# Kernel tuning notes

Measured on AMD Instinct MI355X. Metric: run time of the kernel, lower is better.

Reference implementation:

```python
import jax, jax.numpy as jnp
import numpy as np

N_NODES = 100000
N_EDGES = 1600000
N_GRAPHS = 256
F_IN, F_HID, F_OUT = 32, 64, 64


def setup_inputs() -> dict:
    key = jax.random.key(0)
    ks = jax.random.split(key, 9)
    x = jax.random.normal(ks[0], (N_NODES, F_IN), dtype=jnp.float32)
    edge_index = jax.random.randint(ks[1], (2, N_EDGES), 0, N_NODES, dtype=jnp.int64)
    batch = jnp.sort(jax.random.randint(ks[2], (N_NODES,), 0, N_GRAPHS, dtype=jnp.int64))
    def glorot(k, fan_in, fan_out):
        lim = (6.0 / (fan_in + fan_out)) ** 0.5
        return jax.random.uniform(k, (fan_in, fan_out), jnp.float32, -lim, lim)
    return {
        "x": x,
        "edge_index": edge_index,
        "batch": batch,
        # GraphConv layer 1: lin_rel (with bias) on aggregated msgs, lin_root (no bias) on self
        "W1_rel": glorot(ks[3], F_IN, F_HID),
        "b1_rel": jnp.zeros((F_HID,), jnp.float32),
        "W1_root": glorot(ks[4], F_IN, F_HID),
        # GraphConv layer 2
        "W2_rel": glorot(ks[5], F_HID, F_OUT),
        "b2_rel": jnp.zeros((F_OUT,), jnp.float32),
        "W2_root": glorot(ks[6], F_HID, F_OUT),
    }


def _graph_conv(h, src, dst, W_rel, b_rel, W_root):
    # PyG GraphConv (aggr='add'): out_i = W_rel @ (sum_{j->i} h_j) + b_rel + W_root @ h_i
    agg = jax.ops.segment_sum(h[src], dst, num_segments=N_NODES)  # [N, F]
    return agg @ W_rel + b_rel + h @ W_root


def reference(x, edge_index, batch, W1_rel, b1_rel, W1_root, W2_rel, b2_rel, W2_root):
    src, dst = edge_index[0], edge_index[1]
    h1 = jnp.tanh(_graph_conv(x, src, dst, W1_rel, b1_rel, W1_root))   # [N, 64]
    h2 = jnp.tanh(_graph_conv(h1, src, dst, W2_rel, b2_rel, W2_root))  # [N, 64]
    # global_mean_pool over graph ids
    sums = jax.ops.segment_sum(h2, batch, num_segments=N_GRAPHS)       # [B, 64]
    counts = jax.ops.segment_sum(jnp.ones((h2.shape[0],), h2.dtype), batch, num_segments=N_GRAPHS)
    return sums / jnp.maximum(counts, 1.0)[:, None]
```

## Files before the change

### kernel.cpp

```cpp
#include <hip/hip_runtime.h>

#define N_NODES 100000
#define N_EDGES 1600000
#define N_GRAPHS 256
#define F_IN 32
#define F_HID 64
#define F_OUT 64

#define T_WAVES 8192
#define NODES_PER_WAVE ((N_NODES + T_WAVES - 1) / T_WAVES)
#define FILL_PASS_SHIFT 14
#define FILL_NPASS ((N_NODES + (1 << FILL_PASS_SHIFT) - 1) >> FILL_PASS_SHIFT)

__global__ void histogram_dst(const int* __restrict__ dst, int* __restrict__ deg) {
    int e = blockIdx.x * blockDim.x + threadIdx.x;
    if (e < N_EDGES) atomicAdd(&deg[dst[e]], 1);
}

__global__ void scan1(const int* __restrict__ deg, int* __restrict__ end_, int* __restrict__ partials) {
    __shared__ int s[256];
    int tid = threadIdx.x;
    int i = blockIdx.x * 256 + tid;
    int v = (i < N_NODES) ? deg[i] : 0;
    s[tid] = v;
    __syncthreads();
#pragma unroll
    for (int off = 1; off < 256; off <<= 1) {
        int t = 0;
        if (tid >= off) t = s[tid - off];
        __syncthreads();
        if (tid >= off) s[tid] += t;
        __syncthreads();
    }
    if (i < N_NODES) end_[i] = s[tid];
    if (tid == 255) partials[blockIdx.x] = s[255];
}

__global__ void scan2(int* __restrict__ partials, int nb) {
    __shared__ int s[512];
    int tid = threadIdx.x;
    int v = (tid < nb) ? partials[tid] : 0;
    s[tid] = v;
    __syncthreads();
#pragma unroll
    for (int off = 1; off < 512; off <<= 1) {
        int t = 0;
        if (tid >= off) t = s[tid - off];
        __syncthreads();
        if (tid >= off) s[tid] += t;
        __syncthreads();
    }
    int excl = (tid > 0) ? s[tid - 1] : 0;
    if (tid < nb) partials[tid] = excl;
}

__global__ void scan3(const int* __restrict__ deg, int* __restrict__ end_,
                      int* __restrict__ cursor, const int* __restrict__ partials) {
    int i = blockIdx.x * 256 + threadIdx.x;
    if (i < N_NODES) {
        int e = end_[i] + partials[blockIdx.x];
        end_[i] = e;
        cursor[i] = e - deg[i];
    }
}

__global__ __launch_bounds__(256) void fill_adj_mp(const int* __restrict__ src,
                                                   const int* __restrict__ dst,
                                                   int* __restrict__ cursor,
                                                   int* __restrict__ adj) {
    int gid = blockIdx.x * blockDim.x + threadIdx.x;
    int stride = gridDim.x * blockDim.x;
    for (int p = 0; p < FILL_NPASS; ++p) {
        for (int e = gid; e < N_EDGES; e += stride) {
            int d = dst[e];
            if ((d >> FILL_PASS_SHIFT) == p) {
                int pos = atomicAdd(&cursor[d], 1);
                adj[pos] = src[e];
            }
        }
    }
}

__global__ __launch_bounds__(256) void gather64_v2(const float* __restrict__ h,
        const int* __restrict__ adj, const int* __restrict__ end_, const int* __restrict__ deg,
        float* __restrict__ agg) {
    int node = (blockIdx.x * blockDim.x + threadIdx.x) >> 6;
    int lane = threadIdx.x & 63;
    if (node >= N_NODES) return;
    int e = end_[node];
    int d = deg[node];
    int s = e - d;
    int q = lane & 15;
    int r = lane >> 4;
    const float4* h4 = (const float4*)h;

    float ax = 0.f, ay = 0.f, az = 0.f, aw = 0.f;
    for (int base = 0; base < d; base += 8) {
        int i0 = base + r;
        int i1 = base + 4 + r;
        if (i0 < d) {
            int s0 = adj[s + i0];
            float4 v = h4[(size_t)s0 * 16 + q];
            ax += v.x; ay += v.y; az += v.z; aw += v.w;
        }
        if (i1 < d) {
            int s1 = adj[s + i1];
            float4 v = h4[(size_t)s1 * 16 + q];
            ax += v.x; ay += v.y; az += v.z; aw += v.w;
        }
    }
#pragma unroll
    for (int off = 16; off < 64; off <<= 1) {
        ax += __shfl_xor(ax, off);
        ay += __shfl_xor(ay, off);
        az += __shfl_xor(az, off);
        aw += __shfl_xor(aw, off);
    }
    if (r == 0) {
        float4 o; o.x = ax; o.y = ay; o.z = az; o.w = aw;
        ((float4*)agg)[(size_t)node * 16 + q] = o;
    }
}

__global__ __launch_bounds__(256) void gather32_v2(const float* __restrict__ xin,
        const int* __restrict__ adj, const int* __restrict__ end_, const int* __restrict__ deg,
        float* __restrict__ agg) {
    int node = (blockIdx.x * blockDim.x + threadIdx.x) >> 6;
    int lane = threadIdx.x & 63;
    if (node >= N_NODES) return;
    int e = end_[node];
    int d = deg[node];
    int s = e - d;
    int q = lane & 7;
    int r = lane >> 3;
    const float4* x4 = (const float4*)xin;

    float ax = 0.f, ay = 0.f, az = 0.f, aw = 0.f;
    for (int base = 0; base < d; base += 16) {
        int i0 = base + r;
        int i1 = base + 8 + r;
        if (i0 < d) {
            int s0 = adj[s + i0];
            float4 v = x4[(size_t)s0 * 8 + q];
            ax += v.x; ay += v.y; az += v.z; aw += v.w;
        }
        if (i1 < d) {
            int s1 = adj[s + i1];
            float4 v = x4[(size_t)s1 * 8 + q];
            ax += v.x; ay += v.y; az += v.z; aw += v.w;
        }
    }
#pragma unroll
    for (int off = 8; off < 64; off <<= 1) {
        ax += __shfl_xor(ax, off);
        ay += __shfl_xor(ay, off);
        az += __shfl_xor(az, off);
        aw += __shfl_xor(aw, off);
    }
    if (r == 0) {
        float4 o; o.x = ax; o.y = ay; o.z = az; o.w = aw;
        ((float4*)agg)[(size_t)node * 8 + q] = o;
    }
}

__global__ __launch_bounds__(256) void transform1_reg(const float* __restrict__ agg,
        const float* __restrict__ xin,
        const float* __restrict__ Wrel, const float* __restrict__ brel,
        const float* __restrict__ Wroot,
        float* __restrict__ h1) {
    int lane = threadIdx.x & 63;
    int wgid = __builtin_amdgcn_readfirstlane(blockIdx.x * 4 + (threadIdx.x >> 6));
    int n0 = wgid * NODES_PER_WAVE;
    if (n0 >= N_NODES) return;
    int n1 = min(n0 + NODES_PER_WAVE, N_NODES);

    float wrel[32], wroot[32];
#pragma unroll
    for (int k = 0; k < 32; ++k) {
        wrel[k] = Wrel[k * 64 + lane];
        wroot[k] = Wroot[k * 64 + lane];
    }
    float b = brel[lane];

    for (int node = n0; node < n1; ++node) {
        const float4* ar = (const float4*)(agg + (size_t)node * 32);
        const float4* xr = (const float4*)(xin + (size_t)node * 32);
        float o = b;
#pragma unroll
        for (int kk = 0; kk < 8; ++kk) {
            float4 a4 = ar[kk];
            float4 x4 = xr[kk];
            o += a4.x * wrel[kk * 4 + 0] + a4.y * wrel[kk * 4 + 1]
               + a4.z * wrel[kk * 4 + 2] + a4.w * wrel[kk * 4 + 3];
            o += x4.x * wroot[kk * 4 + 0] + x4.y * wroot[kk * 4 + 1]
               + x4.z * wroot[kk * 4 + 2] + x4.w * wroot[kk * 4 + 3];
        }
        h1[(size_t)node * 64 + lane] = tanhf(o);
    }
}

__global__ __launch_bounds__(256) void transform2_pool_reg(const float* __restrict__ agg,
        const float* __restrict__ h1,
        const float* __restrict__ Wrel, const float* __restrict__ brel,
        const float* __restrict__ Wroot,
        const int* __restrict__ batch,
        float* __restrict__ sums) {
    int lane = threadIdx.x & 63;
    int wgid = __builtin_amdgcn_readfirstlane(blockIdx.x * 4 + (threadIdx.x >> 6));
    int n0 = wgid * NODES_PER_WAVE;
    if (n0 >= N_NODES) return;
    int n1 = min(n0 + NODES_PER_WAVE, N_NODES);

    float wrel[64], wroot[64];
#pragma unroll
    for (int k = 0; k < 64; ++k) {
        wrel[k] = Wrel[k * 64 + lane];
        wroot[k] = Wroot[k * 64 + lane];
    }
    float b = brel[lane];

    float psum = 0.0f;
    int curg = batch[n0];
    for (int node = n0; node < n1; ++node) {
        const float4* ar = (const float4*)(agg + (size_t)node * 64);
        const float4* xr = (const float4*)(h1 + (size_t)node * 64);
        float o = b;
#pragma unroll
        for (int kk = 0; kk < 16; ++kk) {
            float4 a4 = ar[kk];
            float4 x4 = xr[kk];
            o += a4.x * wrel[kk * 4 + 0] + a4.y * wrel[kk * 4 + 1]
               + a4.z * wrel[kk * 4 + 2] + a4.w * wrel[kk * 4 + 3];
            o += x4.x * wroot[kk * 4 + 0] + x4.y * wroot[kk * 4 + 1]
               + x4.z * wroot[kk * 4 + 2] + x4.w * wroot[kk * 4 + 3];
        }
        float h2 = tanhf(o);
        int g = batch[node];
        if (g != curg) {
            atomicAdd(&sums[(size_t)curg * 64 + lane], psum);
            psum = 0.0f;
            curg = g;
        }
        psum += h2;
    }
    atomicAdd(&sums[(size_t)curg * 64 + lane], psum);
}

__global__ void graph_counts(const int* __restrict__ batch, float* __restrict__ counts) {
    int g = threadIdx.x;
    if (g >= N_GRAPHS) return;
    int lo = 0, hi = N_NODES;
    while (lo < hi) { int mid = (lo + hi) >> 1; if (batch[mid] < g) lo = mid + 1; else hi = mid; }
    int start = lo;
    lo = 0; hi = N_NODES;
    while (lo < hi) { int mid = (lo + hi) >> 1; if (batch[mid] <= g) lo = mid + 1; else hi = mid; }
    counts[g] = (float)(lo - start);
}

__global__ void finalize(const float* __restrict__ sums,
                         const float* __restrict__ counts,
                         float* __restrict__ out) {
    int i = blockIdx.x * blockDim.x + threadIdx.x;
    if (i < N_GRAPHS * 64) {
        float c = counts[i >> 6];
        out[i] = sums[i] / fmaxf(c, 1.0f);
    }
}

extern "C" void kernel_launch(void* const* d_in, const int* in_sizes, int n_in,
                              void* d_out, int out_size, void* d_ws, size_t ws_size,
                              hipStream_t stream) {
    const float* x       = (const float*)d_in[0];
    const int*   ei      = (const int*)d_in[1];
    const int*   batch   = (const int*)d_in[2];
    const float* W1_rel  = (const float*)d_in[3];
    const float* b1_rel  = (const float*)d_in[4];
    const float* W1_root = (const float*)d_in[5];
    const float* W2_rel  = (const float*)d_in[6];
    const float* b2_rel  = (const float*)d_in[7];
    const float* W2_root = (const float*)d_in[8];
    float* out = (float*)d_out;

    const int* src = ei;
    const int* dst = ei + N_EDGES;

    char* ws = (char*)d_ws;
    int*   deg      = (int*)(ws + 0);
    float* sums     = (float*)(ws + 400000);
    float* counts   = (float*)(ws + 465536);
    int*   end_     = (int*)(ws + 466560);
    int*   cursor   = (int*)(ws + 866560);
    int*   partials = (int*)(ws + 1266560);
    int*   adj      = (int*)(ws + 1268608);
    float* aggbuf   = (float*)(ws + 7668608);
    float* h1       = (float*)(ws + 33268608);

    hipMemsetAsync(d_ws, 0, 466560, stream);

    const int NB_NODE = (N_NODES + 255) / 256;
    histogram_dst<<<(N_EDGES + 255) / 256, 256, 0, stream>>>(dst, deg);
    scan1<<<NB_NODE, 256, 0, stream>>>(deg, end_, partials);
    scan2<<<1, 512, 0, stream>>>(partials, NB_NODE);
    scan3<<<NB_NODE, 256, 0, stream>>>(deg, end_, cursor, partials);
    fill_adj_mp<<<2048, 256, 0, stream>>>(src, dst, cursor, adj);

    gather32_v2<<<(N_NODES * 64 + 255) / 256, 256, 0, stream>>>(x, adj, end_, deg, aggbuf);
    transform1_reg<<<T_WAVES / 4, 256, 0, stream>>>(aggbuf, x, W1_rel, b1_rel, W1_root, h1);

    gather64_v2<<<(N_NODES * 64 + 255) / 256, 256, 0, stream>>>(h1, adj, end_, deg, aggbuf);
    transform2_pool_reg<<<T_WAVES / 4, 256, 0, stream>>>(aggbuf, h1, W2_rel, b2_rel, W2_root, batch, sums);

    graph_counts<<<1, 256, 0, stream>>>(batch, counts);
    finalize<<<(N_GRAPHS * 64 + 255) / 256, 256, 0, stream>>>(sums, counts, out);
}
```

Before: 384.8 us.

## Partition histogram and adjacency fill by destination range per XCD

The destination-degree histogram and CSR fill kernels now split destination nodes into 8 ranges, one per XCD. Each block is assigned a range by its block index, assuming round-robin block dispatch across XCDs, so the atomics for a node range stay in one XCD's L2. This replaces the earlier multi-pass fill, which scanned all edges several times. Every edge list is now read once per XCD (8 times in total), with nontemporal loads to limit cache pollution. The trade is more redundant reads of edge data for more local atomics.

```diff
diff --git a/kernel.cpp b/kernel.cpp
--- a/kernel.cpp
+++ b/kernel.cpp
@@ -9,12 +9,20 @@
 
 #define T_WAVES 8192
 #define NODES_PER_WAVE ((N_NODES + T_WAVES - 1) / T_WAVES)
-#define FILL_PASS_SHIFT 14
-#define FILL_NPASS ((N_NODES + (1 << FILL_PASS_SHIFT) - 1) >> FILL_PASS_SHIFT)
-
-__global__ void histogram_dst(const int* __restrict__ dst, int* __restrict__ deg) {
-    int e = blockIdx.x * blockDim.x + threadIdx.x;
-    if (e < N_EDGES) atomicAdd(&deg[dst[e]], 1);
+#define NXCD 8
+#define DPX ((N_NODES + NXCD - 1) / NXCD)
+
+__global__ __launch_bounds__(256) void histogram_xcd(const int* __restrict__ dst,
+                                                     int* __restrict__ deg) {
+    int xcd = blockIdx.x & (NXCD - 1);
+    int sub = blockIdx.x >> 3;
+    int nsub = gridDim.x >> 3;
+    int d_lo = xcd * DPX;
+    int d_hi = min(d_lo + DPX, N_NODES);
+    for (int e = sub * blockDim.x + threadIdx.x; e < N_EDGES; e += nsub * blockDim.x) {
+        int d = __builtin_nontemporal_load(dst + e);
+        if (d >= d_lo && d < d_hi) atomicAdd(&deg[d], 1);
+    }
 }
 
 __global__ void scan1(const int* __restrict__ deg, int* __restrict__ end_, int* __restrict__ partials) {
@@ -64,19 +72,20 @@
     }
 }
 
-__global__ __launch_bounds__(256) void fill_adj_mp(const int* __restrict__ src,
-                                                   const int* __restrict__ dst,
-                                                   int* __restrict__ cursor,
-                                                   int* __restrict__ adj) {
-    int gid = blockIdx.x * blockDim.x + threadIdx.x;
-    int stride = gridDim.x * blockDim.x;
-    for (int p = 0; p < FILL_NPASS; ++p) {
-        for (int e = gid; e < N_EDGES; e += stride) {
-            int d = dst[e];
-            if ((d >> FILL_PASS_SHIFT) == p) {
-                int pos = atomicAdd(&cursor[d], 1);
-                adj[pos] = src[e];
-            }
+__global__ __launch_bounds__(256) void fill_adj_xcd(const int* __restrict__ src,
+                                                    const int* __restrict__ dst,
+                                                    int* __restrict__ cursor,
+                                                    int* __restrict__ adj) {
+    int xcd = blockIdx.x & (NXCD - 1);
+    int sub = blockIdx.x >> 3;
+    int nsub = gridDim.x >> 3;
+    int d_lo = xcd * DPX;
+    int d_hi = min(d_lo + DPX, N_NODES);
+    for (int e = sub * blockDim.x + threadIdx.x; e < N_EDGES; e += nsub * blockDim.x) {
+        int d = __builtin_nontemporal_load(dst + e);
+        if (d >= d_lo && d < d_hi) {
+            int pos = atomicAdd(&cursor[d], 1);
+            adj[pos] = __builtin_nontemporal_load(src + e);
         }
     }
 }
@@ -298,11 +307,11 @@
     hipMemsetAsync(d_ws, 0, 466560, stream);
 
     const int NB_NODE = (N_NODES + 255) / 256;
-    histogram_dst<<<(N_EDGES + 255) / 256, 256, 0, stream>>>(dst, deg);
+    histogram_xcd<<<2048, 256, 0, stream>>>(dst, deg);
     scan1<<<NB_NODE, 256, 0, stream>>>(deg, end_, partials);
     scan2<<<1, 512, 0, stream>>>(partials, NB_NODE);
     scan3<<<NB_NODE, 256, 0, stream>>>(deg, end_, cursor, partials);
-    fill_adj_mp<<<2048, 256, 0, stream>>>(src, dst, cursor, adj);
+    fill_adj_xcd<<<2048, 256, 0, stream>>>(src, dst, cursor, adj);
 
     gather32_v2<<<(N_NODES * 64 + 255) / 256, 256, 0, stream>>>(x, adj, end_, deg, aggbuf);
     transform1_reg<<<T_WAVES / 4, 256, 0, stream>>>(aggbuf, x, W1_rel, b1_rel, W1_root, h1);
```

After: 374.9 us. 1.03x faster.
